# Performance work log

Hardware: AMD Instinct MI355X
Metric: run time of the kernel (lower is better)

Reference implementation:

```python
import jax, jax.numpy as jnp
import numpy as np

EMB = 512
HEADS = 8
QKV = 512
WIN = 256  # 'range' init arg, >1 so W = range


def setup_inputs() -> dict:
    key = jax.random.key(0)
    ks = jax.random.split(key, 9)
    B, N = 2, 4096
    s_in = 1.0 / np.sqrt(EMB)
    s_qkv = 1.0 / np.sqrt(QKV)
    return {
        "x": jax.random.normal(ks[0], (B, N, EMB), jnp.float32),
        "Wq": jax.random.normal(ks[1], (EMB, QKV), jnp.float32) * s_in,
        "bq": jnp.zeros((QKV,), jnp.float32),
        "Wk": jax.random.normal(ks[2], (EMB, QKV), jnp.float32) * s_in,
        "bk": jnp.zeros((QKV,), jnp.float32),
        "Wv": jax.random.normal(ks[3], (EMB, QKV), jnp.float32) * s_in,
        "bv": jnp.zeros((QKV,), jnp.float32),
        "Wfc": jax.random.normal(ks[4], (QKV, EMB), jnp.float32) * s_qkv,
        "bfc": jnp.zeros((EMB,), jnp.float32),
    }


def reference(x, Wq, bq, Wk, bk, Wv, bv, Wfc, bfc):
    B, N, E = x.shape
    hd = QKV // HEADS  # head dim = 64
    # window mask: |i-j| <= W//2 -> 0 else -inf
    idx = jnp.arange(N)
    inwin = jnp.abs(idx[None, :] - idx[:, None]) <= (WIN // 2)
    M = jnp.where(inwin, 0.0, -jnp.inf).astype(x.dtype)  # [N,N]

    def split(h):  # [B,N,QKV] -> [B,H,N,hd]
        return h.reshape(B, N, HEADS, hd).transpose(0, 2, 1, 3)

    q = split(x @ Wq + bq)
    k = split(x @ Wk + bk)
    v = split(x @ Wv + bv)

    scale = 1.0 / np.sqrt(hd)
    attn = jnp.einsum("bhnd,bhmd->bhnm", q, k) * scale + M
    attn = jax.nn.softmax(attn, axis=-1)
    o = jnp.einsum("bhnm,bhmd->bhnd", attn, v)  # [B,H,N,hd]
    o = o.transpose(0, 2, 1, 3).reshape(B, N, QKV)
    return o @ Wfc + bfc
```

## Files before the change

### kernel.cpp

```cpp
#include <hip/hip_runtime.h>
#include <math.h>

typedef __bf16 bf16;
typedef __attribute__((ext_vector_type(8))) __bf16 bf16x8;
typedef __attribute__((ext_vector_type(4))) float f32x4;

#define N_SEQ 4096
#define NEGINF -1e30f

__device__ __forceinline__ void gl_lds16(const void* g, void* l) {
    __builtin_amdgcn_global_load_lds(
        (const __attribute__((address_space(1))) void*)g,
        (__attribute__((address_space(3))) void*)l, 16, 0, 0);
}

__device__ __forceinline__ bf16x8 frag64(const bf16* base, int row, int g) {
    return *(const bf16x8*)(base + (row << 6) + ((g ^ (row & 7)) << 3));
}

__global__ __launch_bounds__(256) void cast_x_k(const float* __restrict__ x,
                                                bf16* __restrict__ xb) {
    int idx = blockIdx.x * 256 + threadIdx.x;
    const float4* xv = (const float4*)x;
    float4 a = xv[idx * 2], b = xv[idx * 2 + 1];
    bf16x8 o;
    o[0] = (bf16)a.x; o[1] = (bf16)a.y; o[2] = (bf16)a.z; o[3] = (bf16)a.w;
    o[4] = (bf16)b.x; o[5] = (bf16)b.y; o[6] = (bf16)b.z; o[7] = (bf16)b.w;
    ((bf16x8*)xb)[idx] = o;
}

__global__ __launch_bounds__(256) void transpose_w_k(
    const float* __restrict__ W0, const float* __restrict__ W1,
    const float* __restrict__ W2, const float* __restrict__ W3,
    bf16* __restrict__ T0, bf16* __restrict__ T1,
    bf16* __restrict__ T2, bf16* __restrict__ T3) {
    const int z = blockIdx.z;
    const float* W = (z == 0) ? W0 : (z == 1) ? W1 : (z == 2) ? W2 : W3;
    bf16* T = (z == 0) ? T0 : (z == 1) ? T1 : (z == 2) ? T2 : T3;
    __shared__ bf16 tile[64][65];
    const int t = threadIdx.x;
    const int k0 = blockIdx.x << 6, n0 = blockIdx.y << 6;
#pragma unroll
    for (int i = 0; i < 16; i++) {
        int idx = (i << 8) + t;
        int r = idx >> 6, c = idx & 63;
        tile[r][c] = (bf16)W[(size_t)(k0 + r) * 512 + n0 + c];
    }
    __syncthreads();
#pragma unroll
    for (int i = 0; i < 16; i++) {
        int idx = (i << 8) + t;
        int r = idx >> 6, c = idx & 63;
        T[(size_t)(n0 + r) * 512 + k0 + c] = tile[c][r];
    }
}

template <int OUT>
__global__ __launch_bounds__(256) void gemm_bf16_k(
    const bf16* __restrict__ A, const bf16* __restrict__ Bt,
    const float* __restrict__ bias, void* __restrict__ Cout) {
    __shared__ bf16 sA[2][8192];
    __shared__ bf16 sB[2][8192];
    const int t = threadIdx.x;
    const int lane = t & 63, wid = t >> 6;
    const int wr = wid >> 1, wc = wid & 1;
    const int m0 = blockIdx.x << 7, n0 = blockIdx.y << 7;

    f32x4 acc[4][4] = {};

    const bf16* Ag = A + ((size_t)m0 << 9);
    const bf16* Bg = Bt + ((size_t)n0 << 9);

#pragma unroll
    for (int i = 0; i < 4; i++) {
        int gid = (i << 8) + t;
        int row = gid >> 3, gs = ((gid & 7) ^ (row & 7)) << 3;
        gl_lds16(Ag + ((size_t)row << 9) + gs, &sA[0][gid << 3]);
        gl_lds16(Bg + ((size_t)row << 9) + gs, &sB[0][gid << 3]);
    }
    __syncthreads();

    int buf = 0;
    for (int kt = 0; kt < 8; kt++) {
        if (kt < 7) {
            int k0 = (kt + 1) << 6;
#pragma unroll
            for (int i = 0; i < 4; i++) {
                int gid = (i << 8) + t;
                int row = gid >> 3, gs = ((gid & 7) ^ (row & 7)) << 3;
                gl_lds16(Ag + ((size_t)row << 9) + k0 + gs, &sA[buf ^ 1][gid << 3]);
                gl_lds16(Bg + ((size_t)row << 9) + k0 + gs, &sB[buf ^ 1][gid << 3]);
            }
        }
#pragma unroll
        for (int ks = 0; ks < 2; ks++) {
            int g = (ks << 2) + (lane >> 4);
            bf16x8 af[4], bfr[4];
#pragma unroll
            for (int mi = 0; mi < 4; mi++)
                af[mi] = frag64(&sA[buf][0], (wr << 6) + (mi << 4) + (lane & 15), g);
#pragma unroll
            for (int ni = 0; ni < 4; ni++)
                bfr[ni] = frag64(&sB[buf][0], (wc << 6) + (ni << 4) + (lane & 15), g);
#pragma unroll
            for (int mi = 0; mi < 4; mi++)
#pragma unroll
                for (int ni = 0; ni < 4; ni++)
                    acc[mi][ni] = __builtin_amdgcn_mfma_f32_16x16x32_bf16(
                        af[mi], bfr[ni], acc[mi][ni], 0, 0, 0);
        }
        __syncthreads();
        buf ^= 1;
    }

#pragma unroll
    for (int mi = 0; mi < 4; mi++) {
#pragma unroll
        for (int ni = 0; ni < 4; ni++) {
            int grow0 = m0 + (wr << 6) + (mi << 4) + ((lane >> 4) << 2);
            int gcol = n0 + (wc << 6) + (ni << 4) + (lane & 15);
            float bb = bias[gcol];
#pragma unroll
            for (int r = 0; r < 4; r++) {
                int grow = grow0 + r;
                float v = acc[mi][ni][r] + bb;
                if (OUT == 0) {
                    int b = grow >> 12, n = grow & 4095;
                    int h = gcol >> 6, d = gcol & 63;
                    size_t idx = ((size_t)(((b << 3) + h) * 4096 + n) << 6) + d;
                    ((bf16*)Cout)[idx] = (bf16)v;
                } else if (OUT == 1) {
                    ((bf16*)Cout)[((size_t)grow << 9) + gcol] = (bf16)v;
                } else {
                    ((float*)Cout)[((size_t)grow << 9) + gcol] = v;
                }
            }
        }
    }
}

__global__ __launch_bounds__(256) void attn_bf16_k(
    const bf16* __restrict__ Q, const bf16* __restrict__ K,
    const bf16* __restrict__ V, bf16* __restrict__ O) {
    __shared__ bf16 QP[4096];
    __shared__ bf16 Ks[4096];
    __shared__ bf16 VT[4096];

    const int t = threadIdx.x;
    const int lane = t & 63, wid = t >> 6;
    const int bh = blockIdx.x >> 6;
    const int q0 = (blockIdx.x & 63) << 6;

    const bf16* Qp = Q + ((size_t)bh << 18);
    const bf16* Kp = K + ((size_t)bh << 18);
    const bf16* Vp = V + ((size_t)bh << 18);

#pragma unroll
    for (int i = 0; i < 2; i++) {
        int gid = (i << 8) + t;
        int row = gid >> 3, gs = ((gid & 7) ^ (row & 7)) << 3;
        gl_lds16(Qp + ((size_t)(q0 + row) << 6) + gs, &QP[gid << 3]);
    }
    __syncthreads();

    bf16x8 aq[2];
#pragma unroll
    for (int ks = 0; ks < 2; ks++)
        aq[ks] = frag64(QP, (wid << 4) + (lane & 15), (ks << 2) + (lane >> 4));

    float mrun[4], lrun[4];
    f32x4 acc_o[4] = {};
#pragma unroll
    for (int r = 0; r < 4; r++) { mrun[r] = NEGINF; lrun[r] = 0.f; }

    const int cstart = (q0 >= 128) ? q0 - 128 : 0;
    const int cend = (q0 + 192 <= N_SEQ) ? q0 + 192 : N_SEQ;
    bf16* Pw = &QP[wid << 10];

    for (int c0 = cstart; c0 < cend; c0 += 64) {
        __syncthreads();
#pragma unroll
        for (int i = 0; i < 2; i++) {
            int gid = (i << 8) + t;
            int row = gid >> 3, gs = ((gid & 7) ^ (row & 7)) << 3;
            gl_lds16(Kp + ((size_t)(c0 + row) << 6) + gs, &Ks[gid << 3]);
        }
        {
            int key = t >> 2;
            int gd0 = (t & 3) << 1;
            const uint4* vs = (const uint4*)(Vp + ((size_t)(c0 + key) << 6));
            union { uint4 u; bf16 h[8]; } u0, u1;
            u0.u = vs[gd0]; u1.u = vs[gd0 + 1];
#pragma unroll
            for (int e = 0; e < 8; e++) {
                int d0 = (gd0 << 3) + e;
                VT[(d0 << 6) + (((key >> 3) ^ (d0 & 7)) << 3) + (key & 7)] = u0.h[e];
                int d1 = d0 + 8;
                VT[(d1 << 6) + (((key >> 3) ^ (d1 & 7)) << 3) + (key & 7)] = u1.h[e];
            }
        }
        __syncthreads();

        f32x4 s[4] = {};
#pragma unroll
        for (int ks = 0; ks < 2; ks++) {
            int g = (ks << 2) + (lane >> 4);
#pragma unroll
            for (int ni = 0; ni < 4; ni++) {
                bf16x8 bk = frag64(Ks, (ni << 4) + (lane & 15), g);
                s[ni] = __builtin_amdgcn_mfma_f32_16x16x32_bf16(aq[ks], bk, s[ni], 0, 0, 0);
            }
        }

#pragma unroll
        for (int r = 0; r < 4; r++) {
            int rowl = ((lane >> 4) << 2) + r;
            int qi = q0 + (wid << 4) + rowl;
            float v[4];
#pragma unroll
            for (int ni = 0; ni < 4; ni++) {
                int kj = c0 + (ni << 4) + (lane & 15);
                int dd = qi - kj;
                v[ni] = (dd <= 128 && dd >= -128) ? s[ni][r] * 0.125f : NEGINF;
            }
            float mx = fmaxf(fmaxf(v[0], v[1]), fmaxf(v[2], v[3]));
#pragma unroll
            for (int off = 1; off < 16; off <<= 1)
                mx = fmaxf(mx, __shfl_xor(mx, off));
            float mn = fmaxf(mrun[r], mx);
            float alpha = __expf(mrun[r] - mn);
            float rs = 0.f;
#pragma unroll
            for (int ni = 0; ni < 4; ni++) {
                float p = __expf(v[ni] - mn);
                rs += p;
                int col = (ni << 4) + (lane & 15);
                Pw[(rowl << 6) + (((col >> 3) ^ (rowl & 7)) << 3) + (col & 7)] = (bf16)p;
            }
#pragma unroll
            for (int off = 1; off < 16; off <<= 1)
                rs += __shfl_xor(rs, off);
            mrun[r] = mn;
            lrun[r] = lrun[r] * alpha + rs;
#pragma unroll
            for (int nd = 0; nd < 4; nd++) acc_o[nd][r] *= alpha;
        }

#pragma unroll
        for (int ks = 0; ks < 2; ks++) {
            int g = (ks << 2) + (lane >> 4);
            bf16x8 pa = frag64(Pw, lane & 15, g);
#pragma unroll
            for (int nd = 0; nd < 4; nd++) {
                bf16x8 bv = frag64(VT, (nd << 4) + (lane & 15), g);
                acc_o[nd] = __builtin_amdgcn_mfma_f32_16x16x32_bf16(pa, bv, acc_o[nd], 0, 0, 0);
            }
        }
    }

    const int b = bh >> 3, h = bh & 7;
    float inv[4];
#pragma unroll
    for (int r = 0; r < 4; r++) inv[r] = 1.f / lrun[r];
#pragma unroll
    for (int nd = 0; nd < 4; nd++) {
#pragma unroll
        for (int r = 0; r < 4; r++) {
            int n = q0 + (wid << 4) + ((lane >> 4) << 2) + r;
            int d = (nd << 4) + (lane & 15);
            O[(((size_t)(b * 4096 + n)) << 9) + (h << 6) + d] =
                (bf16)(acc_o[nd][r] * inv[r]);
        }
    }
}

extern "C" void kernel_launch(void* const* d_in, const int* in_sizes, int n_in,
                              void* d_out, int out_size, void* d_ws, size_t ws_size,
                              hipStream_t stream) {
    (void)in_sizes; (void)n_in; (void)out_size; (void)ws_size;
    const float* x   = (const float*)d_in[0];
    const float* Wq  = (const float*)d_in[1];
    const float* bq  = (const float*)d_in[2];
    const float* Wk  = (const float*)d_in[3];
    const float* bk  = (const float*)d_in[4];
    const float* Wv  = (const float*)d_in[5];
    const float* bv  = (const float*)d_in[6];
    const float* Wfc = (const float*)d_in[7];
    const float* bfc = (const float*)d_in[8];

    bf16* xb  = (bf16*)d_ws;
    bf16* Wtq = xb + (size_t)8192 * 512;
    bf16* Wtk = Wtq + 512 * 512;
    bf16* Wtv = Wtk + 512 * 512;
    bf16* Wtf = Wtv + 512 * 512;
    bf16* Qb  = Wtf + 512 * 512;
    bf16* Kb  = Qb + (size_t)16 * 4096 * 64;
    bf16* Vb  = Kb + (size_t)16 * 4096 * 64;
    bf16* Ob  = Vb + (size_t)16 * 4096 * 64;

    cast_x_k<<<(8192 * 512) / (256 * 8), 256, 0, stream>>>(x, xb);
    transpose_w_k<<<dim3(8, 8, 4), 256, 0, stream>>>(Wq, Wk, Wv, Wfc,
                                                     Wtq, Wtk, Wtv, Wtf);
    dim3 gg(64, 4);
    gemm_bf16_k<0><<<gg, 256, 0, stream>>>(xb, Wtq, bq, Qb);
    gemm_bf16_k<0><<<gg, 256, 0, stream>>>(xb, Wtk, bk, Kb);
    gemm_bf16_k<0><<<gg, 256, 0, stream>>>(xb, Wtv, bv, Vb);
    attn_bf16_k<<<1024, 256, 0, stream>>>(Qb, Kb, Vb, Ob);
    gemm_bf16_k<2><<<gg, 256, 0, stream>>>(Ob, Wtf, bfc, d_out);
}
```

Before: 155.3 us.

## Fuse Q/K/V projections into one GEMM and narrow output GEMM tile

```diff
diff --git a/kernel.cpp b/kernel.cpp
--- a/kernel.cpp
+++ b/kernel.cpp
@@ -29,96 +29,101 @@
     ((bf16x8*)xb)[idx] = o;
 }
 
-__global__ __launch_bounds__(256) void transpose_w_k(
-    const float* __restrict__ W0, const float* __restrict__ W1,
-    const float* __restrict__ W2, const float* __restrict__ W3,
-    bf16* __restrict__ T0, bf16* __restrict__ T1,
-    bf16* __restrict__ T2, bf16* __restrict__ T3) {
-    const int z = blockIdx.z;
-    const float* W = (z == 0) ? W0 : (z == 1) ? W1 : (z == 2) ? W2 : W3;
-    bf16* T = (z == 0) ? T0 : (z == 1) ? T1 : (z == 2) ? T2 : T3;
-    __shared__ bf16 tile[64][65];
+__global__ __launch_bounds__(256) void prep_w_k(
+    const float* __restrict__ Wq, const float* __restrict__ bq,
+    const float* __restrict__ Wk, const float* __restrict__ bk,
+    const float* __restrict__ Wv, const float* __restrict__ bv,
+    const float* __restrict__ Wfc, const float* __restrict__ bfc,
+    bf16* __restrict__ Wcat, float* __restrict__ bcat) {
     const int t = threadIdx.x;
     const int k0 = blockIdx.x << 6, n0 = blockIdx.y << 6;
+    const int sel = n0 >> 9, nloc = n0 & 511;
+    const float* W = (sel == 0) ? Wq : (sel == 1) ? Wk : (sel == 2) ? Wv : Wfc;
+    const float* bi = (sel == 0) ? bq : (sel == 1) ? bk : (sel == 2) ? bv : bfc;
+    __shared__ bf16 tile[64][65];
 #pragma unroll
     for (int i = 0; i < 16; i++) {
         int idx = (i << 8) + t;
         int r = idx >> 6, c = idx & 63;
-        tile[r][c] = (bf16)W[(size_t)(k0 + r) * 512 + n0 + c];
+        tile[r][c] = (bf16)W[(size_t)(k0 + r) * 512 + nloc + c];
     }
     __syncthreads();
 #pragma unroll
     for (int i = 0; i < 16; i++) {
         int idx = (i << 8) + t;
         int r = idx >> 6, c = idx & 63;
-        T[(size_t)(n0 + r) * 512 + k0 + c] = tile[c][r];
-    }
-}
-
-template <int OUT>
+        Wcat[(size_t)(n0 + r) * 512 + k0 + c] = tile[c][r];
+    }
+    if (blockIdx.x == 0 && t < 64) bcat[n0 + t] = bi[nloc + t];
+}
+
+template <int OUT, int BN>
 __global__ __launch_bounds__(256) void gemm_bf16_k(
     const bf16* __restrict__ A, const bf16* __restrict__ Bt,
     const float* __restrict__ bias, void* __restrict__ Cout) {
-    __shared__ bf16 sA[2][8192];
-    __shared__ bf16 sB[2][8192];
+    constexpr int NI = BN / 32;
+    constexpr int BIT = BN / 32;
+    __shared__ bf16 sA[2][128 * 64];
+    __shared__ bf16 sB[2][BN * 64];
     const int t = threadIdx.x;
     const int lane = t & 63, wid = t >> 6;
     const int wr = wid >> 1, wc = wid & 1;
-    const int m0 = blockIdx.x << 7, n0 = blockIdx.y << 7;
-
-    f32x4 acc[4][4] = {};
+    const int m0 = blockIdx.x << 7;
+    const int n0 = blockIdx.y * BN;
+
+    f32x4 acc[4][NI] = {};
 
     const bf16* Ag = A + ((size_t)m0 << 9);
     const bf16* Bg = Bt + ((size_t)n0 << 9);
 
-#pragma unroll
-    for (int i = 0; i < 4; i++) {
-        int gid = (i << 8) + t;
-        int row = gid >> 3, gs = ((gid & 7) ^ (row & 7)) << 3;
-        gl_lds16(Ag + ((size_t)row << 9) + gs, &sA[0][gid << 3]);
-        gl_lds16(Bg + ((size_t)row << 9) + gs, &sB[0][gid << 3]);
-    }
+#define STAGE(buf, k0)                                                      \
+    {                                                                       \
+        _Pragma("unroll") for (int i = 0; i < 4; i++) {                     \
+            int gid = (i << 8) + t;                                         \
+            int row = gid >> 3, gs = ((gid & 7) ^ (row & 7)) << 3;          \
+            gl_lds16(Ag + ((size_t)row << 9) + (k0) + gs, &sA[buf][gid << 3]); \
+        }                                                                   \
+        _Pragma("unroll") for (int i = 0; i < BIT; i++) {                   \
+            int gid = (i << 8) + t;                                         \
+            int row = gid >> 3, gs = ((gid & 7) ^ (row & 7)) << 3;          \
+            gl_lds16(Bg + ((size_t)row << 9) + (k0) + gs, &sB[buf][gid << 3]); \
+        }                                                                   \
+    }
+
+    STAGE(0, 0);
     __syncthreads();
 
     int buf = 0;
     for (int kt = 0; kt < 8; kt++) {
-        if (kt < 7) {
-            int k0 = (kt + 1) << 6;
-#pragma unroll
-            for (int i = 0; i < 4; i++) {
-                int gid = (i << 8) + t;
-                int row = gid >> 3, gs = ((gid & 7) ^ (row & 7)) << 3;
-                gl_lds16(Ag + ((size_t)row << 9) + k0 + gs, &sA[buf ^ 1][gid << 3]);
-                gl_lds16(Bg + ((size_t)row << 9) + k0 + gs, &sB[buf ^ 1][gid << 3]);
-            }
-        }
+        if (kt < 7) STAGE(buf ^ 1, (kt + 1) << 6);
 #pragma unroll
         for (int ks = 0; ks < 2; ks++) {
             int g = (ks << 2) + (lane >> 4);
-            bf16x8 af[4], bfr[4];
+            bf16x8 af[4], bfr[NI];
 #pragma unroll
             for (int mi = 0; mi < 4; mi++)
                 af[mi] = frag64(&sA[buf][0], (wr << 6) + (mi << 4) + (lane & 15), g);
 #pragma unroll
-            for (int ni = 0; ni < 4; ni++)
-                bfr[ni] = frag64(&sB[buf][0], (wc << 6) + (ni << 4) + (lane & 15), g);
+            for (int ni = 0; ni < NI; ni++)
+                bfr[ni] = frag64(&sB[buf][0], wc * (BN / 2) + (ni << 4) + (lane & 15), g);
 #pragma unroll
             for (int mi = 0; mi < 4; mi++)
 #pragma unroll
-                for (int ni = 0; ni < 4; ni++)
+                for (int ni = 0; ni < NI; ni++)
                     acc[mi][ni] = __builtin_amdgcn_mfma_f32_16x16x32_bf16(
                         af[mi], bfr[ni], acc[mi][ni], 0, 0, 0);
         }
         __syncthreads();
         buf ^= 1;
     }
+#undef STAGE
 
 #pragma unroll
     for (int mi = 0; mi < 4; mi++) {
 #pragma unroll
-        for (int ni = 0; ni < 4; ni++) {
+        for (int ni = 0; ni < NI; ni++) {
             int grow0 = m0 + (wr << 6) + (mi << 4) + ((lane >> 4) << 2);
-            int gcol = n0 + (wc << 6) + (ni << 4) + (lane & 15);
+            int gcol = n0 + wc * (BN / 2) + (ni << 4) + (lane & 15);
             float bb = bias[gcol];
 #pragma unroll
             for (int r = 0; r < 4; r++) {
@@ -126,11 +131,11 @@
                 float v = acc[mi][ni][r] + bb;
                 if (OUT == 0) {
                     int b = grow >> 12, n = grow & 4095;
-                    int h = gcol >> 6, d = gcol & 63;
-                    size_t idx = ((size_t)(((b << 3) + h) * 4096 + n) << 6) + d;
+                    int sel = gcol >> 9, rem = gcol & 511;
+                    int h = rem >> 6, d = rem & 63;
+                    size_t idx =
+                        (((size_t)((sel << 4) + (b << 3) + h) * 4096 + n) << 6) + d;
                     ((bf16*)Cout)[idx] = (bf16)v;
-                } else if (OUT == 1) {
-                    ((bf16*)Cout)[((size_t)grow << 9) + gcol] = (bf16)v;
                 } else {
                     ((float*)Cout)[((size_t)grow << 9) + gcol] = v;
                 }
@@ -288,23 +293,23 @@
     const float* Wfc = (const float*)d_in[7];
     const float* bfc = (const float*)d_in[8];
 
-    bf16* xb  = (bf16*)d_ws;
-    bf16* Wtq = xb + (size_t)8192 * 512;
-    bf16* Wtk = Wtq + 512 * 512;
-    bf16* Wtv = Wtk + 512 * 512;
-    bf16* Wtf = Wtv + 512 * 512;
-    bf16* Qb  = Wtf + 512 * 512;
-    bf16* Kb  = Qb + (size_t)16 * 4096 * 64;
-    bf16* Vb  = Kb + (size_t)16 * 4096 * 64;
-    bf16* Ob  = Vb + (size_t)16 * 4096 * 64;
+    bf16* xb    = (bf16*)d_ws;
+    bf16* Wcat  = xb + (size_t)8192 * 512;
+    float* bcat = (float*)(Wcat + (size_t)2048 * 512);
+    bf16* QKVb  = (bf16*)(bcat + 2048);
+    bf16* Ob    = QKVb + (size_t)3 * 16 * 4096 * 64;
 
     cast_x_k<<<(8192 * 512) / (256 * 8), 256, 0, stream>>>(x, xb);
-    transpose_w_k<<<dim3(8, 8, 4), 256, 0, stream>>>(Wq, Wk, Wv, Wfc,
-                                                     Wtq, Wtk, Wtv, Wtf);
-    dim3 gg(64, 4);
-    gemm_bf16_k<0><<<gg, 256, 0, stream>>>(xb, Wtq, bq, Qb);
-    gemm_bf16_k<0><<<gg, 256, 0, stream>>>(xb, Wtk, bk, Kb);
-    gemm_bf16_k<0><<<gg, 256, 0, stream>>>(xb, Wtv, bv, Vb);
+    prep_w_k<<<dim3(8, 32), 256, 0, stream>>>(Wq, bq, Wk, bk, Wv, bv, Wfc, bfc,
+                                              Wcat, bcat);
+
+    gemm_bf16_k<0, 128><<<dim3(64, 12), 256, 0, stream>>>(xb, Wcat, bcat, QKVb);
+
+    const bf16* Qb = QKVb;
+    const bf16* Kb = QKVb + ((size_t)1 << 22);
+    const bf16* Vb = QKVb + ((size_t)2 << 22);
     attn_bf16_k<<<1024, 256, 0, stream>>>(Qb, Kb, Vb, Ob);
-    gemm_bf16_k<2><<<gg, 256, 0, stream>>>(Ob, Wtf, bfc, d_out);
-}
+
+    gemm_bf16_k<1, 64><<<dim3(64, 8), 256, 0, stream>>>(
+        Ob, Wcat + ((size_t)1536 << 9), bcat + 1536, d_out);
+}
```

Measured after the change: 148.1 us. -4.7%, faster.
